# Optimization experiments

Measured on AMD Instinct MI355X. Metric: run time of the kernel, lower is better.

## Reference

```python
import jax, jax.numpy as jnp
import numpy as np

_SAMPLING_EPS = 1e-5


def setup_inputs() -> dict:
    key = jax.random.key(0)
    k1, k2, k3, k4, k5 = jax.random.split(key, 5)
    B, V = 128, 128000
    logits = jax.random.normal(k1, (B, V), dtype=jnp.float32)
    temperature = jax.random.uniform(k2, (B,), dtype=jnp.float32)
    top_k = jax.random.randint(k3, (B,), 0, 1024)
    top_p = jax.random.uniform(k4, (B,), dtype=jnp.float32)
    # uniform noise -> exponential via -log(u) inside reference (torch's q.exponential_())
    q = jnp.clip(jax.random.uniform(k5, (B, V), dtype=jnp.float32), 1e-10, 1.0)
    return {"logits": logits, "temperature": temperature, "top_k": top_k,
            "top_p": top_p, "q": q, "max_num_logprobs": 5}


def reference(logits, temperature, top_k, top_p, q, max_num_logprobs):
    B, V = logits.shape
    # apply_temperature: temp < eps treated as 1.0 (greedy rows untouched)
    temp = jnp.where(temperature < _SAMPLING_EPS, 1.0, temperature)
    logits = logits.astype(jnp.float32) / temp[:, None]

    # _apply_top_k_top_p: ascending sort over vocab
    idx = jnp.argsort(logits, axis=-1)                      # [B, V]
    ls = jnp.take_along_axis(logits, idx, axis=-1)          # sorted ascending
    k = jnp.clip(top_k.astype(jnp.int32), 1, V)
    thr = jnp.take_along_axis(ls, (V - k)[:, None], axis=-1)  # k-th largest value
    ls = jnp.where(ls < thr, -jnp.inf, ls)
    # top-p on the top-k-masked sorted logits
    ps = jax.nn.softmax(ls, axis=-1)
    cum = jnp.cumsum(ps, axis=-1)
    p_mask = cum <= (1.0 - top_p)[:, None]
    p_mask = p_mask.at[:, -1].set(False)
    ls = jnp.where(p_mask, -jnp.inf, ls)
    # scatter masked sorted logits back to original vocab positions
    rows = jnp.arange(B)[:, None]
    logits = jnp.zeros_like(logits).at[rows, idx].set(ls)

    # get_probs + sample
    probs = jax.nn.softmax(logits, axis=-1)
    e = -jnp.log(q)                                         # exponential noise
    greedy = jnp.argmax(probs, axis=-1)
    rand = jnp.argmax(probs / e, axis=-1)                   # Gumbel-max equivalent
    sampled = jnp.where(temperature < _SAMPLING_EPS, greedy, rand).astype(jnp.int32)

    # top-k logprobs
    logprobs = jax.nn.log_softmax(logits, axis=-1)
    topk_logprobs, topk_indices = jax.lax.top_k(logprobs, max_num_logprobs)
    return sampled, topk_logprobs, topk_indices.astype(jnp.int32)
```

## Files before the change

kernel.cpp:

```cpp
#include <hip/hip_runtime.h>
#include <math.h>
#include <float.h>

typedef unsigned long long u64;
typedef unsigned u32;

#define NT 1024
#define NW 16
#define NT1 256
#define NT4 256
#define EPT 8
#define SL 8
#define NB 8192
#define BSH 19
#define CAP 2048
#define TOPN 5
#define SCALE_D 17592186044416.0
#define NEG_BIG -3.0e38f

struct RowCtl { u32 kb; u32 cnt0; u32 pad[30]; };

__device__ __forceinline__ u32 key_of(float f){
  u32 u = __float_as_uint(f);
  return (u & 0x80000000u) ? ~u : (u | 0x80000000u);
}
__device__ __forceinline__ float key_to_float(u32 k){
  u32 u = (k & 0x80000000u) ? (k & 0x7FFFFFFFu) : ~k;
  return __uint_as_float(u);
}
__device__ __forceinline__ u64 quantMass(float l, float m){
  float ef = expf(l - m);
  return (u64)((double)ef * SCALE_D + 0.5);
}

struct Top5 { float v[TOPN]; int ix[TOPN]; };
__device__ __forceinline__ void t5_init(Top5& t){
  for (int j=0;j<TOPN;j++){ t.v[j] = -INFINITY; t.ix[j] = 0x7FFFFFFF; }
}
__device__ __forceinline__ void t5_insert(Top5& t, float nv, int ni){
  for (int j=0;j<TOPN;j++){
    if (nv > t.v[j] || (nv == t.v[j] && ni < t.ix[j])){
      for (int s=TOPN-1;s>j;s--){ t.v[s]=t.v[s-1]; t.ix[s]=t.ix[s-1]; }
      t.v[j]=nv; t.ix[j]=ni;
      return;
    }
  }
}

__device__ void scan_excl(u64* arr, int n, u64* wsum){
  const int tid = threadIdx.x, lane = tid & 63, w = tid >> 6;
  __syncthreads();
  const int chunk = (n + NT - 1) / NT;
  const int base = tid * chunk;
  u64 local = 0;
  for (int j=0;j<chunk;j++){ int i=base+j; if (i<n) local += arr[i]; }
  u64 inc = local;
  for (int off=1; off<64; off<<=1){
    u64 up = __shfl_up(inc, off, 64);
    if (lane >= off) inc += up;
  }
  if (lane == 63) wsum[w] = inc;
  __syncthreads();
  if (tid == 0){
    u64 acc = 0;
    for (int i=0;i<NW;i++){ u64 v = wsum[i]; wsum[i] = acc; acc += v; }
    arr[n] = acc;
  }
  __syncthreads();
  u64 run = wsum[w] + (inc - local);
  for (int j=0;j<chunk;j++){ int i=base+j; if (i<n){ u64 v=arr[i]; arr[i]=run; run += v; } }
  __syncthreads();
}


__global__ void k0_zero(u32* __restrict__ hist, u32* __restrict__ ctlw, int Bn){
  size_t n = (size_t)Bn * NB;
  size_t stride = (size_t)gridDim.x * blockDim.x;
  for (size_t i = (size_t)blockIdx.x*blockDim.x + threadIdx.x; i < n; i += stride) hist[i] = 0;
  size_t nc = (size_t)Bn * (sizeof(RowCtl)/4);
  for (size_t i = (size_t)blockIdx.x*blockDim.x + threadIdx.x; i < nc; i += stride) ctlw[i] = 0;
}

__global__ __launch_bounds__(NT1) void k1_hist(const float* __restrict__ L,
        const float* __restrict__ temp, u32* __restrict__ hist, int Bn, int Vn){
  __shared__ u32 lh[NB];
  const int b = blockIdx.y, s = blockIdx.x, tid = threadIdx.x;
  for (int j=tid;j<NB;j+=NT1) lh[j]=0;
  const float tr = temp[b]; const float tEff = (tr < 1e-5f) ? 1.0f : tr;
  const float* Lr = L + (size_t)b*Vn;
  const int chunk = (Vn + SL-1)/SL;
  const int i0 = s*chunk, i1 = min(i0+chunk, Vn);
  __syncthreads();
  const int nv = (i1 - i0) / 4;
  const float4* L4 = (const float4*)(Lr + i0);
  for (int v=tid; v<nv; v+=NT1){
    float4 x = L4[v];
    #pragma unroll
    for (int e=0;e<4;e++){
      float l = (&x.x)[e] / tEff;
      atomicAdd(&lh[key_of(l)>>BSH], 1u);
    }
  }
  for (int i=i0+nv*4+tid; i<i1; i+=NT1){
    float l = Lr[i]/tEff;
    atomicAdd(&lh[key_of(l)>>BSH], 1u);
  }
  __syncthreads();
  u32* Hr = hist + (size_t)b*NB;
  for (int j=tid;j<NB;j+=NT1){ u32 c = lh[j]; if (c) atomicAdd(&Hr[j], c); }
}

__global__ __launch_bounds__(NT) void k2_kb(const int* __restrict__ top_k,
        const u32* __restrict__ hist, RowCtl* __restrict__ ctl, int Bn, int Vn){
  __shared__ u32 sh[NB+1];
  __shared__ u32 wsum[NW];
  __shared__ int s_g;
  const int b = blockIdx.x, tid = threadIdx.x, lane = tid&63, w = tid>>6;
  const u32* Hr = hist + (size_t)b*NB;
  for (int j=tid;j<NB;j+=NT) sh[j] = Hr[j];
  __syncthreads();
  const int chunk = NB/NT;
  u32 local=0;
  for (int j=0;j<chunk;j++) local += sh[tid*chunk+j];
  u32 inc = local;
  for (int off=1;off<64;off<<=1){ u32 up=__shfl_up(inc,off,64); if (lane>=off) inc+=up; }
  if (lane==63) wsum[w]=inc;
  __syncthreads();
  if (tid==0){ u32 acc=0; for(int i=0;i<NW;i++){u32 v=wsum[i]; wsum[i]=acc; acc+=v;} sh[NB]=acc; }
  __syncthreads();
  u32 run = wsum[w] + (inc - local);
  for (int j=0;j<chunk;j++){ int i2=tid*chunk+j; u32 v=sh[i2]; sh[i2]=run; run+=v; }
  __syncthreads();
  int kk = top_k[b]; if (kk<1) kk=1; if (kk>Vn) kk=Vn;
  const u32 rank = (u32)(Vn - kk);
  for (int j=tid;j<NB;j+=NT) if (sh[j] <= rank && rank < sh[j+1]) s_g = j;
  __syncthreads();
  if (tid==0) ctl[b].kb = (u32)s_g;
}

__global__ __launch_bounds__(NT1) void k3_collect(const float* __restrict__ L,
        const float* __restrict__ temp, u64* __restrict__ cand, RowCtl* __restrict__ ctl,
        int Bn, int Vn){
  const int b = blockIdx.y, s = blockIdx.x, tid = threadIdx.x;
  const float tr = temp[b]; const float tEff = (tr<1e-5f)?1.0f:tr;
  const u32 kbMinKey = ctl[b].kb << BSH;
  const float* Lr = L + (size_t)b*Vn;
  u64* Cr = cand + (size_t)b*CAP;
  const int chunk = (Vn + SL-1)/SL;
  const int i0 = s*chunk, i1 = min(i0+chunk, Vn);
  const int nv = (i1 - i0) / 4;
  const float4* L4 = (const float4*)(Lr + i0);
  const int lane = tid & 63;
  for (int v=tid; v<nv; v+=NT1){
    float4 x = L4[v];
    #pragma unroll
    for (int e=0;e<4;e++){
      float l = (&x.x)[e] / tEff;
      u32 k = key_of(l);
      bool pred = (k >= kbMinKey);
      u64 mk = __ballot(pred);
      if (mk){
        int leader = __ffsll((long long)mk) - 1;
        u32 base = 0;
        if (lane == leader) base = atomicAdd(&ctl[b].cnt0, (u32)__popcll(mk));
        base = __shfl(base, leader, 64);
        if (pred){
          u32 p = base + (u32)__popcll(mk & ((1ull<<lane)-1ull));
          if (p < CAP) Cr[p] = ((u64)k<<32) | (u64)(u32)(i0 + v*4 + e);
        }
      }
    }
  }
  for (int i=i0+nv*4+tid; i<i1; i+=NT1){
    float l = Lr[i]/tEff;
    u32 k = key_of(l);
    if (k >= kbMinKey){
      u32 p = atomicAdd(&ctl[b].cnt0, 1u);
      if (p < CAP) Cr[p] = ((u64)k<<32) | (u64)(u32)i;
    }
  }
}

__global__ __launch_bounds__(NT4) void k4_solve(const float* __restrict__ L,
        const float* __restrict__ temp, const int* __restrict__ top_k,
        const float* __restrict__ top_p, const float* __restrict__ qn,
        const u64* __restrict__ cand, const RowCtl* __restrict__ ctl,
        float* __restrict__ out, int Bn, int Vn){
  __shared__ u64 s_red[2][4];
  __shared__ u32 s_mk;
  __shared__ float s_fill[16];
  __shared__ Top5 s_wt5[NT4/64];
  __shared__ double s_wr[NT4/64];
  __shared__ int s_wri[NT4/64];
  __shared__ int s_wg[NT4/64];

  const int b = blockIdx.x, tid = threadIdx.x, lane = tid&63, w = tid>>6;
  const u32 n0raw = ctl[b].cnt0;
  if (n0raw == 0 || n0raw > CAP) return;
  const int n0 = (int)n0raw;
  const float tr = temp[b]; const float tEff = (tr<1e-5f)?1.0f:tr;
  const float* Lr = L + (size_t)b*Vn;
  const float* Qr = qn + (size_t)b*Vn;
  const u64* Cr = cand + (size_t)b*CAP;
  const u32 kbMinKey = ctl[b].kb << BSH;

  if (tid==0) s_mk = 0;
  if (tid<16) s_fill[tid] = (tid<Vn) ? Lr[tid] : 0.f;
  __syncthreads();
  u32 k_[EPT], ix_[EPT];
  u32 valid = 0;
  u32 mk = 0;
  #pragma unroll
  for (int e=0;e<EPT;e++){
    int p = tid + e*NT4;
    if (p < n0){
      u64 v = Cr[p];
      k_[e] = (u32)(v>>32); ix_[e] = (u32)v;
      valid |= 1u<<e;
      mk = max(mk, k_[e]);
    } else { k_[e]=0u; ix_[e]=0u; }
  }
  for (int off=32; off; off>>=1){ u32 o=__shfl_xor(mk,off,64); mk=max(mk,o); }
  if (lane==0) atomicMax(&s_mk, mk);
  __syncthreads();
  const u32 mKey = s_mk;
  const float m = key_to_float(mKey);
  int buf = 0;

  int kk = top_k[b]; if (kk<1) kk=1; if (kk>Vn) kk=Vn; if (kk>n0) kk=n0;
  u32 rA = (u32)(n0 - kk);
  const u32 xA = kbMinKey ^ mKey;
  const int sbA = xA ? (31 - __clz(xA)) : -1;
  u32 pfx = (sbA==31) ? 0u : (mKey & ((sbA>=0) ? ~((1u<<(sbA+1))-1u) : 0xFFFFFFFFu));
  u32 aA = valid;
  for (int bit=sbA; bit>=0; --bit){
    u32 c0 = 0;
    #pragma unroll
    for (int e=0;e<EPT;e++)
      c0 += ((aA>>e)&1u) & (((k_[e]>>bit)&1u)^1u);
    for (int off=32; off; off>>=1) c0 += __shfl_xor(c0, off, 64);
    if (lane==0) s_red[buf][w] = (u64)c0;
    __syncthreads();
    u32 C0 = (u32)(s_red[buf][0]+s_red[buf][1]+s_red[buf][2]+s_red[buf][3]);
    u32 chosen;
    if (rA < C0) chosen = 0u;
    else { rA -= C0; chosen = 1u; pfx |= (1u<<bit); }
    u32 na = 0;
    #pragma unroll
    for (int e=0;e<EPT;e++)
      na |= (((aA>>e)&1u) & ((((k_[e]>>bit)&1u)==chosen)?1u:0u)) << e;
    aA = na;
    buf ^= 1;
  }
  const u32 thrKey = pfx;

  u64 ms_[EPT];
  u32 aB = 0;
  u64 locT = 0;
  #pragma unroll
  for (int e=0;e<EPT;e++){
    bool sv = ((valid>>e)&1u) && (k_[e] >= thrKey);
    ms_[e] = sv ? quantMass(key_to_float(k_[e]), m) : 0ull;
    if (sv) aB |= 1u<<e;
    locT += ms_[e];
  }
  for (int off=32; off; off>>=1) locT += __shfl_xor(locT, off, 64);
  if (lane==0) s_red[buf][w] = locT;
  __syncthreads();
  const u64 T = s_red[buf][0]+s_red[buf][1]+s_red[buf][2]+s_red[buf][3];
  buf ^= 1;
  const float cf = 1.0f - top_p[b];
  u64 Q = (u64)((double)cf * (double)T);
  if (Q >= T) Q = T - 1;
  const u64 budget = Q;

  const u32 xB = thrKey ^ mKey;
  const int sbB = xB ? (31 - __clz(xB)) : -1;
  u32 pfx2 = (sbB==31) ? 0u : (mKey & ((sbB>=0) ? ~((1u<<(sbB+1))-1u) : 0xFFFFFFFFu));
  for (int bit=sbB; bit>=0; --bit){
    u64 S0 = 0;
    #pragma unroll
    for (int e=0;e<EPT;e++)
      if (((aB>>e)&1u) && !((k_[e]>>bit)&1u)) S0 += ms_[e];
    for (int off=32; off; off>>=1) S0 += __shfl_xor(S0, off, 64);
    if (lane==0) s_red[buf][w] = S0;
    __syncthreads();
    u64 St = s_red[buf][0]+s_red[buf][1]+s_red[buf][2]+s_red[buf][3];
    u32 chosen;
    if (Q < St) chosen = 0u;
    else { Q -= St; chosen = 1u; pfx2 |= (1u<<bit); }
    u32 na = 0;
    #pragma unroll
    for (int e=0;e<EPT;e++)
      na |= (((aB>>e)&1u) & ((((k_[e]>>bit)&1u)==chosen)?1u:0u)) << e;
    aB = na;
    buf ^= 1;
  }
  const u32 vKey = pfx2;
  const u64 qstar = quantMass(key_to_float(vKey), m);
  const u64 tmask = qstar ? (Q / qstar) : 0ull;
  const u64 S2 = T - (budget - Q) - tmask*qstar;

  int idxStar = -1;
  if (tmask > 0){
    u32 r2 = (u32)(tmask - 1);
    u32 aC = 0;
    #pragma unroll
    for (int e=0;e<EPT;e++)
      if (((valid>>e)&1u) && k_[e]==vKey) aC |= 1u<<e;
    const int sbC = 31 - __clz((u32)(Vn-1));
    u32 pfx3 = 0;
    for (int bit=sbC; bit>=0; --bit){
      u32 c0 = 0;
      #pragma unroll
      for (int e=0;e<EPT;e++)
        c0 += ((aC>>e)&1u) & (((ix_[e]>>bit)&1u)^1u);
      for (int off=32; off; off>>=1) c0 += __shfl_xor(c0, off, 64);
      if (lane==0) s_red[buf][w] = (u64)c0;
      __syncthreads();
      u32 C0 = (u32)(s_red[buf][0]+s_red[buf][1]+s_red[buf][2]+s_red[buf][3]);
      u32 chosen;
      if (r2 < C0) chosen = 0u;
      else { r2 -= C0; chosen = 1u; pfx3 |= (1u<<bit); }
      u32 na = 0;
      #pragma unroll
      for (int e=0;e<EPT;e++)
        na |= (((aC>>e)&1u) & ((((ix_[e]>>bit)&1u)==chosen)?1u:0u)) << e;
      aC = na;
      buf ^= 1;
    }
    idxStar = (int)pfx3;
  }

  u32 sv = 0;
  float qv[EPT];
  #pragma unroll
  for (int e=0;e<EPT;e++){
    bool s = ((valid>>e)&1u) &&
             ((k_[e] > vKey) || (k_[e] == vKey && (int)ix_[e] > idxStar));
    if (s) sv |= 1u<<e;
    qv[e] = s ? Qr[ix_[e]] : 1.0f;
  }
  Top5 t5; t5_init(t5);
  double br = -1.0; int bri = 0x7FFFFFFF; int gmin = 0x7FFFFFFF;
  #pragma unroll
  for (int e=0;e<EPT;e++){
    if ((sv>>e)&1u){
      float l = key_to_float(k_[e]); int idx = (int)ix_[e];
      float u = expf(l - m);
      float ee = -logf(qv[e]);
      double ratio = (double)u / (double)ee;
      if (ratio > br || (ratio == br && idx < bri)){ br = ratio; bri = idx; }
      if (k_[e] == mKey && idx < gmin) gmin = idx;
      t5_insert(t5, l, idx);
    }
  }
  for (int off=1; off<64; off<<=1){
    Top5 o;
    for (int j=0;j<TOPN;j++){ o.v[j]=__shfl_xor(t5.v[j],off,64); o.ix[j]=__shfl_xor(t5.ix[j],off,64); }
    for (int j=0;j<TOPN;j++) t5_insert(t5, o.v[j], o.ix[j]);
    double orr = __shfl_xor(br, off, 64); int ori = __shfl_xor(bri, off, 64);
    if (orr > br || (orr == br && ori < bri)){ br = orr; bri = ori; }
    int og = __shfl_xor(gmin, off, 64); if (og < gmin) gmin = og;
  }
  if (lane==0){ s_wt5[w]=t5; s_wr[w]=br; s_wri[w]=bri; s_wg[w]=gmin; }
  __syncthreads();
  if (tid==0){
    Top5 f = s_wt5[0];
    double fr = s_wr[0]; int fri = s_wri[0]; int fg = s_wg[0];
    for (int wi=1; wi<NT4/64; wi++){
      for (int j=0;j<TOPN;j++) t5_insert(f, s_wt5[wi].v[j], s_wt5[wi].ix[j]);
      if (s_wr[wi] > fr || (s_wr[wi]==fr && s_wri[wi]<fri)){ fr=s_wr[wi]; fri=s_wri[wi]; }
      if (s_wg[wi] < fg) fg = s_wg[wi];
    }
    int filled = 0;
    for (int i=0; i<16 && i<Vn && filled<TOPN; i++){
      u32 k2 = key_of(s_fill[i]/tEff);
      bool surv2 = (k2 > vKey) || (k2 == vKey && i > idxStar);
      if (!surv2){ t5_insert(f, -INFINITY, i); filled++; }
    }
    double lS = log((double)S2 / SCALE_D);
    int sampled = (tr < 1e-5f) ? fg : fri;
    out[b] = (float)sampled;
    for (int j=0;j<TOPN;j++){
      float lv = f.v[j];
      float lp = (lv == -INFINITY) ? NEG_BIG : (float)((double)lv - (double)m - lS);
      out[Bn + b*TOPN + j] = lp;
      out[Bn + Bn*TOPN + b*TOPN + j] = (float)f.ix[j];
    }
  }
}


__device__ void find_cross(const u64* arr, int n, u64 target, int* s_fh, u64* s_fb){
  const int tid = threadIdx.x;
  const int chunk = (n + NT - 1) / NT;
  const int base = tid * chunk;
  for (int j=0;j<chunk;j++){
    int i = base + j;
    if (i < n && arr[i] <= target && target < arr[i+1]){ *s_fh = i; *s_fb = arr[i]; }
  }
  __syncthreads();
}

__device__ void fallback_row(int b, const float* logits, const float* temperature,
                             const int* top_k, const float* top_p, const float* qnoise,
                             float* out, int Bn, int Vn){
  __shared__ u64 s_hist[4097];
  __shared__ u64 s_wsum[NW];
  __shared__ int s_fh;
  __shared__ u64 s_fb;
  __shared__ float s_fm[NW];
  __shared__ float s_m;
  __shared__ int s_lastMax;
  __shared__ int s_eqcnt;
  __shared__ int s_eqlist[1024];
  __shared__ int s_sel;
  __shared__ Top5 s_wt5[NW];
  __shared__ double s_wr[NW];
  __shared__ int s_wri[NW];
  __shared__ int s_wg[NW];
  __shared__ u64 s_ws2[NW];

  const int tid = threadIdx.x, lane = tid & 63, w = tid >> 6;
  const float* L  = logits + (size_t)b * Vn;
  const float* Qr = qnoise + (size_t)b * Vn;
  const float tRaw = temperature[b];
  const float tEff = (tRaw < 1e-5f) ? 1.0f : tRaw;

  for (int i=tid;i<4097;i+=NT) s_hist[i] = 0;
  if (tid==0){ s_lastMax = -1; s_eqcnt = 0; }
  __syncthreads();
  float lm = -INFINITY;
  for (int i=tid;i<Vn;i+=NT){
    float l = L[i] / tEff;
    u32 k = key_of(l);
    atomicAdd(&s_hist[k>>20], 1ull);
    lm = fmaxf(lm, l);
  }
  for (int off=32; off; off>>=1) lm = fmaxf(lm, __shfl_xor(lm, off, 64));
  if (lane==0) s_fm[w] = lm;
  scan_excl(s_hist, 4096, s_wsum);
  if (tid==0){ float mm=-INFINITY; for (int i=0;i<NW;i++) mm=fmaxf(mm,s_fm[i]); s_m=mm; }
  __syncthreads();
  const float m = s_m;

  int kk = top_k[b]; if (kk < 1) kk = 1; if (kk > Vn) kk = Vn;
  u64 r = (u64)(Vn - kk);
  find_cross(s_hist, 4096, r, &s_fh, &s_fb);
  const int kb0 = s_fh; r -= s_fb;
  __syncthreads();

  for (int i=tid;i<4097;i+=NT) s_hist[i]=0;
  __syncthreads();
  for (int i=tid;i<Vn;i+=NT){
    float l = L[i]/tEff; u32 k = key_of(l);
    if ((int)(k>>20) == kb0) atomicAdd(&s_hist[(k>>8)&0xFFFu], 1ull);
  }
  scan_excl(s_hist, 4096, s_wsum);
  find_cross(s_hist, 4096, r, &s_fh, &s_fb);
  const int kb1 = s_fh; r -= s_fb;
  __syncthreads();

  const u32 ktop24 = ((u32)kb0<<12) | (u32)kb1;
  for (int i=tid;i<4097;i+=NT) s_hist[i]=0;
  __syncthreads();
  for (int i=tid;i<Vn;i+=NT){
    float l = L[i]/tEff; u32 k = key_of(l);
    if ((k>>8) == ktop24) atomicAdd(&s_hist[k & 0xFFu], 1ull);
  }
  scan_excl(s_hist, 256, s_wsum);
  find_cross(s_hist, 256, r, &s_fh, &s_fb);
  const u32 thrKey = (ktop24<<8) | (u32)s_fh;
  const float thr = key_to_float(thrKey);
  __syncthreads();

  for (int i=tid;i<4097;i+=NT) s_hist[i]=0;
  __syncthreads();
  for (int i=tid;i<Vn;i+=NT){
    float l = L[i]/tEff;
    if (l >= thr){
      u32 k = key_of(l);
      double sd = exp((double)l - (double)m);
      u64 qv = (u64)(sd * SCALE_D + 0.5);
      atomicAdd(&s_hist[k>>20], qv);
      if (l == m) atomicMax(&s_lastMax, i);
    }
  }
  scan_excl(s_hist, 4096, s_wsum);
  const u64 T = s_hist[4096];
  const float cf = 1.0f - top_p[b];
  const double qtd = (double)cf * (double)T;
  u64 Qfix = (qtd >= (double)T) ? T : (u64)qtd;
  const bool allmask = (Qfix >= T);

  u32 vKey = 0xFFFFFFFFu;
  int idxStar = 0x7FFFFFFF;

  if (!allmask){
    find_cross(s_hist, 4096, Qfix, &s_fh, &s_fb);
    const int g0 = s_fh;
    u64 Qrem = Qfix - s_fb;
    __syncthreads();

    for (int i=tid;i<4097;i+=NT) s_hist[i]=0;
    __syncthreads();
    for (int i=tid;i<Vn;i+=NT){
      float l = L[i]/tEff;
      if (l >= thr){
        u32 k = key_of(l);
        if ((int)(k>>20) == g0){
          double sd = exp((double)l - (double)m);
          atomicAdd(&s_hist[(k>>8)&0xFFFu], (u64)(sd*SCALE_D+0.5));
        }
      }
    }
    scan_excl(s_hist, 4096, s_wsum);
    find_cross(s_hist, 4096, Qrem, &s_fh, &s_fb);
    const int g1 = s_fh; Qrem -= s_fb;
    __syncthreads();

    const u32 ptop24 = ((u32)g0<<12)|(u32)g1;
    for (int i=tid;i<4097;i+=NT) s_hist[i]=0;
    __syncthreads();
    for (int i=tid;i<Vn;i+=NT){
      float l = L[i]/tEff;
      if (l >= thr){
        u32 k = key_of(l);
        if ((k>>8) == ptop24){
          double sd = exp((double)l - (double)m);
          atomicAdd(&s_hist[k & 0xFFu], (u64)(sd*SCALE_D+0.5));
        }
      }
    }
    scan_excl(s_hist, 256, s_wsum);
    find_cross(s_hist, 256, Qrem, &s_fh, &s_fb);
    const int g2 = s_fh;
    const u64 base2 = s_fb;
    const u64 nextPref = s_hist[g2+1];
    Qrem -= base2;
    vKey = (ptop24<<8) | (u32)g2;
    const float vStar = key_to_float(vKey);
    const double sv = exp((double)vStar - (double)m);
    const u64 qstar = (u64)(sv*SCALE_D+0.5);
    u64 nstar = (qstar > 0) ? (nextPref - base2) / qstar : 1ull;
    if (nstar < 1) nstar = 1;
    u64 tmask = (qstar > 0) ? (Qrem / qstar) : 0ull;
    if (tmask >= nstar) tmask = nstar - 1;
    idxStar = -1;
    __syncthreads();
    if (tmask >= 1){
      for (int i=tid;i<Vn;i+=NT){
        float l = L[i]/tEff;
        if (key_of(l) == vKey){
          int p = atomicAdd(&s_eqcnt, 1);
          if (p < 1024) s_eqlist[p] = i;
        }
      }
      __syncthreads();
      if (tid == 0){
        int n_ = s_eqcnt; if (n_ > 1024) n_ = 1024;
        for (int a=1;a<n_;a++){
          int key0 = s_eqlist[a]; int c2=a-1;
          while (c2>=0 && s_eqlist[c2]>key0){ s_eqlist[c2+1]=s_eqlist[c2]; c2--; }
          s_eqlist[c2+1]=key0;
        }
        int ti = (int)tmask - 1;
        if (ti >= n_) ti = n_-1;
        s_sel = s_eqlist[ti];
      }
      __syncthreads();
      idxStar = s_sel;
    }
  }

  const int lastMax = s_lastMax;
  Top5 t5; t5_init(t5);
  u64 s2 = 0;
  double br = -1.0; int bri = 0x7FFFFFFF;
  int gmin = 0x7FFFFFFF;
  for (int i=tid;i<Vn;i+=NT){
    float l = L[i]/tEff;
    u32 k = key_of(l);
    bool surv = (l >= thr) &&
                ((k > vKey) || (k == vKey && i > idxStar) || (i == lastMax));
    float val;
    if (surv){
      double sd = exp((double)l - (double)m);
      s2 += (u64)(sd*SCALE_D+0.5);
      float u = expf(l - m);
      float e = -logf(Qr[i]);
      double ratio = (double)u / (double)e;
      if (ratio > br || (ratio == br && i < bri)){ br = ratio; bri = i; }
      if (l == m && i < gmin) gmin = i;
      val = l;
    } else {
      val = -INFINITY;
    }
    t5_insert(t5, val, i);
  }
  for (int off=1; off<64; off<<=1){
    Top5 o;
    for (int j=0;j<TOPN;j++){ o.v[j]=__shfl_xor(t5.v[j],off,64); o.ix[j]=__shfl_xor(t5.ix[j],off,64); }
    for (int j=0;j<TOPN;j++) t5_insert(t5, o.v[j], o.ix[j]);
    double orr = __shfl_xor(br, off, 64);
    int ori = __shfl_xor(bri, off, 64);
    if (orr > br || (orr == br && ori < bri)){ br = orr; bri = ori; }
    int og = __shfl_xor(gmin, off, 64); if (og < gmin) gmin = og;
    s2 += __shfl_xor(s2, off, 64);
  }
  if (lane == 0){
    s_wt5[w] = t5; s_wr[w]=br; s_wri[w]=bri; s_wg[w]=gmin; s_ws2[w]=s2;
  }
  __syncthreads();
  if (tid == 0){
    Top5 f = s_wt5[0];
    double fr = s_wr[0]; int fri = s_wri[0]; int fg = s_wg[0];
    u64 fs2 = s_ws2[0];
    for (int wi=1; wi<NW; wi++){
      for (int j=0;j<TOPN;j++) t5_insert(f, s_wt5[wi].v[j], s_wt5[wi].ix[j]);
      if (s_wr[wi] > fr || (s_wr[wi]==fr && s_wri[wi]<fri)){ fr=s_wr[wi]; fri=s_wri[wi]; }
      if (s_wg[wi] < fg) fg = s_wg[wi];
      fs2 += s_ws2[wi];
    }
    double S2d = (double)fs2 / SCALE_D;
    double lS = log(S2d);
    int sampled = (tRaw < 1e-5f) ? fg : fri;
    out[b] = (float)sampled;
    for (int j=0;j<TOPN;j++){
      float lv = f.v[j];
      float lp = (lv == -INFINITY) ? NEG_BIG : (float)((double)lv - (double)m - lS);
      out[Bn + b*TOPN + j] = lp;
      out[Bn + Bn*TOPN + b*TOPN + j] = (float)f.ix[j];
    }
  }
}

__global__ __launch_bounds__(NT) void k5_rowfb(const float* __restrict__ logits,
        const float* __restrict__ temperature, const int* __restrict__ top_k,
        const float* __restrict__ top_p, const float* __restrict__ qnoise,
        const RowCtl* __restrict__ ctl, float* __restrict__ out, int Bn, int Vn){
  const int b = blockIdx.x;
  const u32 c = ctl[b].cnt0;
  if (c > 0 && c <= CAP) return;
  fallback_row(b, logits, temperature, top_k, top_p, qnoise, out, Bn, Vn);
}

extern "C" __global__ void __launch_bounds__(NT)
sampler_fallback(const float* __restrict__ logits, const float* __restrict__ temperature,
                 const int* __restrict__ top_k, const float* __restrict__ top_p,
                 const float* __restrict__ qnoise, float* __restrict__ out, int Bn, int Vn){
  fallback_row(blockIdx.x, logits, temperature, top_k, top_p, qnoise, out, Bn, Vn);
}


extern "C" void kernel_launch(void* const* d_in, const int* in_sizes, int n_in,
                              void* d_out, int out_size, void* d_ws, size_t ws_size,
                              hipStream_t stream)
{
  const float* logits      = (const float*)d_in[0];
  const float* temperature = (const float*)d_in[1];
  const int*   top_k       = (const int*)d_in[2];
  const float* top_p       = (const float*)d_in[3];
  const float* q           = (const float*)d_in[4];
  const int Bn = in_sizes[1];
  const int Vn = in_sizes[0] / Bn;

  const size_t offCand = (size_t)Bn * NB * 4;
  const size_t offCtl  = offCand + (size_t)Bn * CAP * 8;
  const size_t total   = offCtl + (size_t)Bn * sizeof(RowCtl);

  if (ws_size < total){
    sampler_fallback<<<dim3(Bn), dim3(NT), 0, stream>>>(
        logits, temperature, top_k, top_p, q, (float*)d_out, Bn, Vn);
    return;
  }

  char* wsb = (char*)d_ws;
  u32*    hist = (u32*)wsb;
  u64*    cand = (u64*)(wsb + offCand);
  RowCtl* ctl  = (RowCtl*)(wsb + offCtl);

  k0_zero   <<<dim3(512),     dim3(256), 0, stream>>>(hist, (u32*)ctl, Bn);
  k1_hist   <<<dim3(SL, Bn),  dim3(NT1), 0, stream>>>(logits, temperature, hist, Bn, Vn);
  k2_kb     <<<dim3(Bn),      dim3(NT),  0, stream>>>(top_k, hist, ctl, Bn, Vn);
  k3_collect<<<dim3(SL, Bn),  dim3(NT1), 0, stream>>>(logits, temperature, cand, ctl, Bn, Vn);
  k4_solve  <<<dim3(Bn),      dim3(NT4), 0, stream>>>(logits, temperature, top_k, top_p, q,
                                                      cand, ctl, (float*)d_out, Bn, Vn);
  k5_rowfb  <<<dim3(Bn),      dim3(NT),  0, stream>>>(logits, temperature, top_k, top_p, q,
                                                      ctl, (float*)d_out, Bn, Vn);
}
```

Before: 156.2 us.

## Run per-row solve kernel as a single wavefront with ballot-based radix selects

Shrinks the k4_solve block from four wavefronts to one, so each lane holds 32 candidates and every reduction in the radix selects becomes a wavefront shuffle or ballot/popcount with no shared memory or __syncthreads. The top-k radix select now starts from the known histogram bucket prefix instead of the key range between bucket minimum and row max. The final cross-wave merge and the shared fill buffer are removed. In exchange each row uses fewer threads, more registers per thread, and longer per-lane serial loops over 32 elements.

New measurement: 176.6 us. 1.13x slower.

```diff
diff --git a/kernel.cpp b/kernel.cpp
--- a/kernel.cpp
+++ b/kernel.cpp
@@ -8,12 +8,11 @@
 #define NT 1024
 #define NW 16
 #define NT1 256
-#define NT4 256
-#define EPT 8
 #define SL 8
 #define NB 8192
 #define BSH 19
 #define CAP 2048
+#define EPT 32
 #define TOPN 5
 #define SCALE_D 17592186044416.0
 #define NEG_BIG -3.0e38f
@@ -181,20 +180,12 @@
   }
 }
 
-__global__ __launch_bounds__(NT4) void k4_solve(const float* __restrict__ L,
+__global__ __launch_bounds__(64, 1) void k4_solve(const float* __restrict__ L,
         const float* __restrict__ temp, const int* __restrict__ top_k,
         const float* __restrict__ top_p, const float* __restrict__ qn,
         const u64* __restrict__ cand, const RowCtl* __restrict__ ctl,
         float* __restrict__ out, int Bn, int Vn){
-  __shared__ u64 s_red[2][4];
-  __shared__ u32 s_mk;
-  __shared__ float s_fill[16];
-  __shared__ Top5 s_wt5[NT4/64];
-  __shared__ double s_wr[NT4/64];
-  __shared__ int s_wri[NT4/64];
-  __shared__ int s_wg[NT4/64];
-
-  const int b = blockIdx.x, tid = threadIdx.x, lane = tid&63, w = tid>>6;
+  const int b = blockIdx.x, lane = threadIdx.x;
   const u32 n0raw = ctl[b].cnt0;
   if (n0raw == 0 || n0raw > CAP) return;
   const int n0 = (int)n0raw;
@@ -202,73 +193,59 @@
   const float* Lr = L + (size_t)b*Vn;
   const float* Qr = qn + (size_t)b*Vn;
   const u64* Cr = cand + (size_t)b*CAP;
-  const u32 kbMinKey = ctl[b].kb << BSH;
-
-  if (tid==0) s_mk = 0;
-  if (tid<16) s_fill[tid] = (tid<Vn) ? Lr[tid] : 0.f;
-  __syncthreads();
+  const u32 kb = ctl[b].kb;
+
   u32 k_[EPT], ix_[EPT];
   u32 valid = 0;
   u32 mk = 0;
   #pragma unroll
   for (int e=0;e<EPT;e++){
-    int p = tid + e*NT4;
+    int p = lane + e*64;
     if (p < n0){
       u64 v = Cr[p];
       k_[e] = (u32)(v>>32); ix_[e] = (u32)v;
       valid |= 1u<<e;
       mk = max(mk, k_[e]);
-    } else { k_[e]=0u; ix_[e]=0u; }
-  }
+    } else { k_[e]=0u; ix_[e]=0xFFFFFFFFu; }
+  }
+  #pragma unroll
   for (int off=32; off; off>>=1){ u32 o=__shfl_xor(mk,off,64); mk=max(mk,o); }
-  if (lane==0) atomicMax(&s_mk, mk);
-  __syncthreads();
-  const u32 mKey = s_mk;
+  const u32 mKey = mk;
   const float m = key_to_float(mKey);
-  int buf = 0;
 
   int kk = top_k[b]; if (kk<1) kk=1; if (kk>Vn) kk=Vn; if (kk>n0) kk=n0;
   u32 rA = (u32)(n0 - kk);
-  const u32 xA = kbMinKey ^ mKey;
-  const int sbA = xA ? (31 - __clz(xA)) : -1;
-  u32 pfx = (sbA==31) ? 0u : (mKey & ((sbA>=0) ? ~((1u<<(sbA+1))-1u) : 0xFFFFFFFFu));
-  u32 aA = valid;
-  for (int bit=sbA; bit>=0; --bit){
-    u32 c0 = 0;
-    #pragma unroll
-    for (int e=0;e<EPT;e++)
-      c0 += ((aA>>e)&1u) & (((k_[e]>>bit)&1u)^1u);
-    for (int off=32; off; off>>=1) c0 += __shfl_xor(c0, off, 64);
-    if (lane==0) s_red[buf][w] = (u64)c0;
-    __syncthreads();
-    u32 C0 = (u32)(s_red[buf][0]+s_red[buf][1]+s_red[buf][2]+s_red[buf][3]);
-    u32 chosen;
-    if (rA < C0) chosen = 0u;
-    else { rA -= C0; chosen = 1u; pfx |= (1u<<bit); }
-    u32 na = 0;
-    #pragma unroll
-    for (int e=0;e<EPT;e++)
-      na |= (((aA>>e)&1u) & ((((k_[e]>>bit)&1u)==chosen)?1u:0u)) << e;
-    aA = na;
-    buf ^= 1;
+  u32 pfx = kb << BSH;
+  u32 aA = 0;
+  #pragma unroll
+  for (int e=0;e<EPT;e++)
+    if (((valid>>e)&1u) && (k_[e]>>BSH)==kb) aA |= 1u<<e;
+  for (int bit=BSH-1; bit>=0; --bit){
+    u32 bits = 0;
+    #pragma unroll
+    for (int e=0;e<EPT;e++) bits |= ((k_[e]>>bit)&1u) << e;
+    u32 act0 = aA & ~bits;
+    u32 c = 0;
+    #pragma unroll
+    for (int e=0;e<EPT;e++) c += (u32)__popcll(__ballot((int)((act0>>e)&1u)));
+    if (rA < c) aA = act0;
+    else { rA -= c; aA &= bits; pfx |= (1u<<bit); }
   }
   const u32 thrKey = pfx;
 
   u64 ms_[EPT];
-  u32 aB = 0;
-  u64 locT = 0;
+  u32 aS = 0;
+  u64 T = 0;
   #pragma unroll
   for (int e=0;e<EPT;e++){
     bool sv = ((valid>>e)&1u) && (k_[e] >= thrKey);
     ms_[e] = sv ? quantMass(key_to_float(k_[e]), m) : 0ull;
-    if (sv) aB |= 1u<<e;
-    locT += ms_[e];
-  }
-  for (int off=32; off; off>>=1) locT += __shfl_xor(locT, off, 64);
-  if (lane==0) s_red[buf][w] = locT;
-  __syncthreads();
-  const u64 T = s_red[buf][0]+s_red[buf][1]+s_red[buf][2]+s_red[buf][3];
-  buf ^= 1;
+    if (sv) aS |= 1u<<e;
+    T += ms_[e];
+  }
+  #pragma unroll
+  for (int off=1; off<64; off<<=1) T += __shfl_xor(T, off, 64);
+
   const float cf = 1.0f - top_p[b];
   u64 Q = (u64)((double)cf * (double)T);
   if (Q >= T) Q = T - 1;
@@ -276,25 +253,20 @@
 
   const u32 xB = thrKey ^ mKey;
   const int sbB = xB ? (31 - __clz(xB)) : -1;
-  u32 pfx2 = (sbB==31) ? 0u : (mKey & ((sbB>=0) ? ~((1u<<(sbB+1))-1u) : 0xFFFFFFFFu));
+  u32 pfx2 = (sbB >= 31) ? 0u : (mKey & ~((sbB>=0) ? ((1u<<(sbB+1))-1u) : 0xFFFFFFFFu));
+  u32 aB = aS;
   for (int bit=sbB; bit>=0; --bit){
+    u32 bits = 0;
+    #pragma unroll
+    for (int e=0;e<EPT;e++) bits |= ((k_[e]>>bit)&1u) << e;
+    u32 act0 = aB & ~bits;
     u64 S0 = 0;
     #pragma unroll
-    for (int e=0;e<EPT;e++)
-      if (((aB>>e)&1u) && !((k_[e]>>bit)&1u)) S0 += ms_[e];
-    for (int off=32; off; off>>=1) S0 += __shfl_xor(S0, off, 64);
-    if (lane==0) s_red[buf][w] = S0;
-    __syncthreads();
-    u64 St = s_red[buf][0]+s_red[buf][1]+s_red[buf][2]+s_red[buf][3];
-    u32 chosen;
-    if (Q < St) chosen = 0u;
-    else { Q -= St; chosen = 1u; pfx2 |= (1u<<bit); }
-    u32 na = 0;
-    #pragma unroll
-    for (int e=0;e<EPT;e++)
-      na |= (((aB>>e)&1u) & ((((k_[e]>>bit)&1u)==chosen)?1u:0u)) << e;
-    aB = na;
-    buf ^= 1;
+    for (int e=0;e<EPT;e++) if ((act0>>e)&1u) S0 += ms_[e];
+    #pragma unroll
+    for (int off=1; off<64; off<<=1) S0 += __shfl_xor(S0, off, 64);
+    if (Q < S0) aB = act0;
+    else { Q -= S0; aB &= bits; pfx2 |= (1u<<bit); }
   }
   const u32 vKey = pfx2;
   const u64 qstar = quantMass(key_to_float(vKey), m);
@@ -308,39 +280,33 @@
     #pragma unroll
     for (int e=0;e<EPT;e++)
       if (((valid>>e)&1u) && k_[e]==vKey) aC |= 1u<<e;
-    const int sbC = 31 - __clz((u32)(Vn-1));
     u32 pfx3 = 0;
+    const int sbC = 31 - __clz((u32)((Vn>1)?(Vn-1):1));
     for (int bit=sbC; bit>=0; --bit){
-      u32 c0 = 0;
+      u32 bits = 0;
       #pragma unroll
-      for (int e=0;e<EPT;e++)
-        c0 += ((aC>>e)&1u) & (((ix_[e]>>bit)&1u)^1u);
-      for (int off=32; off; off>>=1) c0 += __shfl_xor(c0, off, 64);
-      if (lane==0) s_red[buf][w] = (u64)c0;
-      __syncthreads();
-      u32 C0 = (u32)(s_red[buf][0]+s_red[buf][1]+s_red[buf][2]+s_red[buf][3]);
-      u32 chosen;
-      if (r2 < C0) chosen = 0u;
-      else { r2 -= C0; chosen = 1u; pfx3 |= (1u<<bit); }
-      u32 na = 0;
+      for (int e=0;e<EPT;e++) bits |= ((ix_[e]>>bit)&1u) << e;
+      u32 act0 = aC & ~bits;
+      u32 c = 0;
       #pragma unroll
-      for (int e=0;e<EPT;e++)
-        na |= (((aC>>e)&1u) & ((((ix_[e]>>bit)&1u)==chosen)?1u:0u)) << e;
-      aC = na;
-      buf ^= 1;
+      for (int e=0;e<EPT;e++) c += (u32)__popcll(__ballot((int)((act0>>e)&1u)));
+      if (r2 < c) aC = act0;
+      else { r2 -= c; aC &= bits; pfx3 |= (1u<<bit); }
     }
     idxStar = (int)pfx3;
   }
 
   u32 sv = 0;
-  float qv[EPT];
   #pragma unroll
   for (int e=0;e<EPT;e++){
     bool s = ((valid>>e)&1u) &&
              ((k_[e] > vKey) || (k_[e] == vKey && (int)ix_[e] > idxStar));
     if (s) sv |= 1u<<e;
-    qv[e] = s ? Qr[ix_[e]] : 1.0f;
-  }
+  }
+  float qv[EPT];
+  #pragma unroll
+  for (int e=0;e<EPT;e++) qv[e] = ((sv>>e)&1u) ? Qr[ix_[e]] : 1.0f;
+
   Top5 t5; t5_init(t5);
   double br = -1.0; int bri = 0x7FFFFFFF; int gmin = 0x7FFFFFFF;
   #pragma unroll
@@ -363,30 +329,23 @@
     if (orr > br || (orr == br && ori < bri)){ br = orr; bri = ori; }
     int og = __shfl_xor(gmin, off, 64); if (og < gmin) gmin = og;
   }
-  if (lane==0){ s_wt5[w]=t5; s_wr[w]=br; s_wri[w]=bri; s_wg[w]=gmin; }
-  __syncthreads();
-  if (tid==0){
-    Top5 f = s_wt5[0];
-    double fr = s_wr[0]; int fri = s_wri[0]; int fg = s_wg[0];
-    for (int wi=1; wi<NT4/64; wi++){
-      for (int j=0;j<TOPN;j++) t5_insert(f, s_wt5[wi].v[j], s_wt5[wi].ix[j]);
-      if (s_wr[wi] > fr || (s_wr[wi]==fr && s_wri[wi]<fri)){ fr=s_wr[wi]; fri=s_wri[wi]; }
-      if (s_wg[wi] < fg) fg = s_wg[wi];
-    }
-    int filled = 0;
-    for (int i=0; i<16 && i<Vn && filled<TOPN; i++){
-      u32 k2 = key_of(s_fill[i]/tEff);
-      bool surv2 = (k2 > vKey) || (k2 == vKey && i > idxStar);
-      if (!surv2){ t5_insert(f, -INFINITY, i); filled++; }
+  if (lane==0){
+    if (t5.v[TOPN-1] == -INFINITY){
+      int filled = 0;
+      for (int i=0; i<16 && i<Vn && filled<TOPN; i++){
+        u32 k2 = key_of(Lr[i]/tEff);
+        bool surv2 = (k2 > vKey) || (k2 == vKey && i > idxStar);
+        if (!surv2){ t5_insert(t5, -INFINITY, i); filled++; }
+      }
     }
     double lS = log((double)S2 / SCALE_D);
-    int sampled = (tr < 1e-5f) ? fg : fri;
+    int sampled = (tr < 1e-5f) ? gmin : bri;
     out[b] = (float)sampled;
     for (int j=0;j<TOPN;j++){
-      float lv = f.v[j];
+      float lv = t5.v[j];
       float lp = (lv == -INFINITY) ? NEG_BIG : (float)((double)lv - (double)m - lS);
       out[Bn + b*TOPN + j] = lp;
-      out[Bn + Bn*TOPN + b*TOPN + j] = (float)f.ix[j];
+      out[Bn + Bn*TOPN + b*TOPN + j] = (float)t5.ix[j];
     }
   }
 }
@@ -685,7 +644,7 @@
   k1_hist   <<<dim3(SL, Bn),  dim3(NT1), 0, stream>>>(logits, temperature, hist, Bn, Vn);
   k2_kb     <<<dim3(Bn),      dim3(NT),  0, stream>>>(top_k, hist, ctl, Bn, Vn);
   k3_collect<<<dim3(SL, Bn),  dim3(NT1), 0, stream>>>(logits, temperature, cand, ctl, Bn, Vn);
-  k4_solve  <<<dim3(Bn),      dim3(NT4), 0, stream>>>(logits, temperature, top_k, top_p, q,
+  k4_solve  <<<dim3(Bn),      dim3(64),  0, stream>>>(logits, temperature, top_k, top_p, q,
                                                       cand, ctl, (float*)d_out, Bn, Vn);
   k5_rowfb  <<<dim3(Bn),      dim3(NT),  0, stream>>>(logits, temperature, top_k, top_p, q,
                                                       ctl, (float*)d_out, Bn, Vn);
```
